# Optimization experiments

Measured on AMD Instinct MI355X. Metric: run time of the kernel, lower is better.

## Reference

```python
import jax, jax.numpy as jnp
import numpy as np

N = 50000
E = 800000
IN_C, HID_C, OUT_C = 128, 128, 64


def setup_inputs() -> dict:
    key = jax.random.key(0)
    k1, k2, k3, k4 = jax.random.split(key, 4)
    x = jax.random.normal(k1, (N, IN_C), dtype=jnp.float32)
    edge_index = jax.random.randint(k2, (2, E), 0, N, dtype=jnp.int32)
    # Glorot-ish init for the two linear layers (PyG GCNConv uses glorot)
    W1 = jax.random.normal(k3, (IN_C, HID_C), dtype=jnp.float32) / np.sqrt(IN_C)
    b1 = jnp.zeros((HID_C,), dtype=jnp.float32)
    W2 = jax.random.normal(k4, (HID_C, OUT_C), dtype=jnp.float32) / np.sqrt(HID_C)
    b2 = jnp.zeros((OUT_C,), dtype=jnp.float32)
    return {"x": x, "edge_index": edge_index, "W1": W1, "b1": b1, "W2": W2, "b2": b2}


def _gcn_norm(edge_index, num_nodes):
    # Add self-loops, then symmetric normalization deg^{-1/2}[row]*deg^{-1/2}[col]
    loop = jnp.arange(num_nodes, dtype=edge_index.dtype)
    row = jnp.concatenate([edge_index[0], loop])  # [E+N] source
    col = jnp.concatenate([edge_index[1], loop])  # [E+N] destination
    deg = jax.ops.segment_sum(jnp.ones_like(col, dtype=jnp.float32), col,
                              num_segments=num_nodes)
    deg_isqrt = jax.lax.rsqrt(deg)  # deg >= 1 due to self-loops
    norm = deg_isqrt[row] * deg_isqrt[col]  # [E+N]
    return row, col, norm


def _gcn_conv(x, row, col, norm, W, b, num_nodes):
    x = x @ W                                   # [N, C_out]
    msg = x[row] * norm[:, None]                # gather + scale, [E+N, C_out]
    out = jax.ops.segment_sum(msg, col, num_segments=num_nodes)  # scatter-add
    return out + b


def reference(x, edge_index, W1, b1, W2, b2):
    num_nodes = x.shape[0]
    row, col, norm = _gcn_norm(edge_index, num_nodes)
    h = _gcn_conv(x, row, col, norm, W1, b1, num_nodes)
    h = jax.nn.relu(h)
    out = _gcn_conv(h, row, col, norm, W2, b2, num_nodes)
    return out
```

## Files before the change

kernel.cpp:

```cpp
#include <hip/hip_runtime.h>


typedef float f32x4 __attribute__((ext_vector_type(4)));
typedef short bf16x8 __attribute__((ext_vector_type(8)));

#define EPB 4096

__device__ inline float bf2f(unsigned short u) {
    return __uint_as_float(((unsigned int)u) << 16);
}
__device__ inline unsigned short f2bf(float f) {
    unsigned int x = __float_as_uint(f);
    x = x + 0x7FFFu + ((x >> 16) & 1u);
    return (unsigned short)(x >> 16);
}
__device__ inline float4 cvt4(ushort4 u) {
    return make_float4(bf2f(u.x), bf2f(u.y), bf2f(u.z), bf2f(u.w));
}

__global__ __launch_bounds__(256) void k_rhist(const int* __restrict__ col,
                                               int* __restrict__ hist,
                                               int e, int nbR, int nbB) {
    __shared__ int h[256];
    int t = threadIdx.x;
    h[t] = 0;
    __syncthreads();
    int base = blockIdx.x * EPB;
#pragma unroll
    for (int i = 0; i < EPB / 256; ++i) {
        int idx = base + t + i * 256;
        if (idx < e) atomicAdd(&h[col[idx] >> 8], 1);
    }
    __syncthreads();
    if (t < nbB) hist[t * nbR + blockIdx.x] = h[t];
}

__global__ __launch_bounds__(256) void k_scan1g(const int* __restrict__ src,
                                                int* __restrict__ dst,
                                                int* __restrict__ bsum, int m) {
    __shared__ int s[256];
    int t = threadIdx.x;
    int i = blockIdx.x * 256 + t;
    int v = (i < m) ? src[i] : 0;
    s[t] = v;
    __syncthreads();
#pragma unroll
    for (int off = 1; off < 256; off <<= 1) {
        int u = (t >= off) ? s[t - off] : 0;
        __syncthreads();
        s[t] += u;
        __syncthreads();
    }
    if (i < m) dst[i] = s[t] - v;
    if (t == 255) bsum[blockIdx.x] = s[255];
}

__global__ __launch_bounds__(256) void k_scan2(int* __restrict__ bsum, int nb) {
    __shared__ int s[256];
    int t = threadIdx.x;
    int v = (t < nb) ? bsum[t] : 0;
    s[t] = v;
    __syncthreads();
#pragma unroll
    for (int off = 1; off < 256; off <<= 1) {
        int u = (t >= off) ? s[t - off] : 0;
        __syncthreads();
        s[t] += u;
        __syncthreads();
    }
    if (t < nb) bsum[t] = s[t] - v;
}

__global__ __launch_bounds__(256) void k_scanaddg(int* __restrict__ dst,
                                                  const int* __restrict__ bsum, int m) {
    int i = blockIdx.x * 256 + threadIdx.x;
    if (i < m) dst[i] += bsum[blockIdx.x];
}

__global__ __launch_bounds__(256) void k_rscatter(const int* __restrict__ row,
                                                  const int* __restrict__ col,
                                                  const int* __restrict__ histscan,
                                                  unsigned int* __restrict__ tmp,
                                                  int e, int nbR, int nbB) {
    __shared__ int base[256];
    __shared__ int h[256];
    int t = threadIdx.x;
    base[t] = (t < nbB) ? histscan[t * nbR + blockIdx.x] : 0;
    h[t] = 0;
    __syncthreads();
    int b0 = blockIdx.x * EPB;
#pragma unroll
    for (int i = 0; i < EPB / 256; ++i) {
        int idx = b0 + t + i * 256;
        if (idx < e) {
            int c = col[idx];
            int bin = c >> 8;
            int rk = atomicAdd(&h[bin], 1);
            tmp[base[bin] + rk] =
                ((unsigned int)(c & 255) << 16) | (unsigned int)row[idx];
        }
    }
}

__global__ __launch_bounds__(256) void k_bsort(const unsigned int* __restrict__ tmp,
                                               const int* __restrict__ histscan,
                                               int* __restrict__ indptr,
                                               float* __restrict__ dinv,
                                               unsigned short* __restrict__ srcidx,
                                               int n, int e, int nbR, int nbB) {
    __shared__ int cnt[256];
    __shared__ int pre[256];
    int b = blockIdx.x;
    int t = threadIdx.x;
    int beg = histscan[b * nbR];
    int end = (b + 1 < nbB) ? histscan[(b + 1) * nbR] : e;

    cnt[t] = 0;
    __syncthreads();
    for (int i = beg + t; i < end; i += 256) atomicAdd(&cnt[tmp[i] >> 16], 1);
    __syncthreads();
    int v = cnt[t];
    pre[t] = v;
    __syncthreads();
#pragma unroll
    for (int off = 1; off < 256; off <<= 1) {
        int u = (t >= off) ? pre[t - off] : 0;
        __syncthreads();
        pre[t] += u;
        __syncthreads();
    }
    int myexcl = pre[t] - v;
    int node = b * 256 + t;
    if (node < n) {
        indptr[node] = beg + myexcl;
        dinv[node] = rsqrtf((float)v + 1.0f);
    }
    if (b == nbB - 1 && t == 0) indptr[n] = e;
    __syncthreads();
    pre[t] = beg + myexcl;
    cnt[t] = 0;
    __syncthreads();
    for (int i = beg + t; i < end; i += 256) {
        unsigned int u = tmp[i];
        int cl = u >> 16;
        int rk = atomicAdd(&cnt[cl], 1);
        srcidx[pre[cl] + rk] = (unsigned short)(u & 0xFFFFu);
    }
}

__global__ __launch_bounds__(256) void k_prepw(const float* __restrict__ W1,
                                               const float* __restrict__ W2,
                                               unsigned short* __restrict__ Wt1,
                                               unsigned short* __restrict__ Wt2) {
    int i = blockIdx.x * 256 + threadIdx.x;
    if (i < 16384) {
        int k = i >> 7, nc = i & 127;
        Wt1[nc * 128 + k] = f2bf(W1[i]);
    } else if (i < 16384 + 8192) {
        int i2 = i - 16384;
        int k = i2 >> 6, nc = i2 & 63;
        Wt2[nc * 128 + k] = f2bf(W2[i2]);
    }
}

__global__ __launch_bounds__(256, 2) void k_gemm1(const float* __restrict__ x,
                                                  const unsigned short* __restrict__ Wt,
                                                  const float* __restrict__ dinv,
                                                  unsigned short* __restrict__ hs, int n) {
    __shared__ unsigned short Xs[128 * 136];
    __shared__ unsigned short Ws[128 * 136];
    __shared__ float dinv_s[128];
    int t = threadIdx.x;
    int r0blk = blockIdx.x * 128;

#pragma unroll
    for (int i = 0; i < 8; ++i) {
        int c = t + i * 256;
        int nc = c >> 4;
        int k0 = (c & 15) * 8;
        bf16x8 v = *(const bf16x8*)&Wt[nc * 128 + k0];
        *(bf16x8*)&Ws[nc * 136 + k0] = v;
    }
#pragma unroll
    for (int i = 0; i < 16; ++i) {
        int c = t + i * 256;
        int r = c >> 5;
        int kq = c & 31;
        float4 v = make_float4(0.f, 0.f, 0.f, 0.f);
        int gr = r0blk + r;
        if (gr < n) v = ((const float4*)x)[gr * 32 + kq];
        ushort4 o;
        o.x = f2bf(v.x); o.y = f2bf(v.y); o.z = f2bf(v.z); o.w = f2bf(v.w);
        *(ushort4*)&Xs[r * 136 + kq * 4] = o;
    }
    if (t < 128) {
        int gr = r0blk + t;
        dinv_s[t] = (gr < n) ? dinv[gr] : 0.f;
    }
    __syncthreads();

    int lane = t & 63, wave = t >> 6;
    int lrow = lane & 15;
    int lk = (lane >> 4) * 8;

    f32x4 acc[2][8];
#pragma unroll
    for (int mi = 0; mi < 2; ++mi)
#pragma unroll
        for (int ni = 0; ni < 8; ++ni) acc[mi][ni] = (f32x4){0.f, 0.f, 0.f, 0.f};

#pragma unroll
    for (int ks = 0; ks < 4; ++ks) {
        int kk = ks * 32 + lk;
        bf16x8 a0 = *(bf16x8*)&Xs[(wave * 32 + lrow) * 136 + kk];
        bf16x8 a1 = *(bf16x8*)&Xs[(wave * 32 + 16 + lrow) * 136 + kk];
#pragma unroll
        for (int ni = 0; ni < 8; ++ni) {
            bf16x8 b = *(bf16x8*)&Ws[(ni * 16 + lrow) * 136 + kk];
            acc[0][ni] = __builtin_amdgcn_mfma_f32_16x16x32_bf16(a0, b, acc[0][ni], 0, 0, 0);
            acc[1][ni] = __builtin_amdgcn_mfma_f32_16x16x32_bf16(a1, b, acc[1][ni], 0, 0, 0);
        }
    }

    int rq = (lane >> 4) * 4;
#pragma unroll
    for (int mi = 0; mi < 2; ++mi)
#pragma unroll
        for (int r = 0; r < 4; ++r) {
            int lrw = wave * 32 + mi * 16 + rq + r;
            int grow = r0blk + lrw;
            if (grow < n) {
                float dv = dinv_s[lrw];
#pragma unroll
                for (int ni = 0; ni < 8; ++ni)
                    hs[grow * 128 + ni * 16 + lrow] = f2bf(acc[mi][ni][r] * dv);
            }
        }
}

__global__ __launch_bounds__(256) void k_gather1(const int* __restrict__ indptr,
                                                 const unsigned short* __restrict__ srcidx,
                                                 const unsigned short* __restrict__ hs,
                                                 const float* __restrict__ dinv,
                                                 const float* __restrict__ b1,
                                                 unsigned short* __restrict__ h1, int n) {
    int wid = (blockIdx.x * 256 + threadIdx.x) >> 6;
    if (wid >= n) return;
    int lane = threadIdx.x & 63;
    int half = lane >> 5;
    int hl = lane & 31;
    const ushort4* hv = (const ushort4*)hs;

    int beg = indptr[wid], end = indptr[wid + 1];
    float4 a0 = make_float4(0.f, 0.f, 0.f, 0.f), a1 = a0, a2 = a0, a3 = a0;

    int j = beg;
    for (; j + 7 < end; j += 8) {
        int sA = srcidx[j + half];
        int sB = srcidx[j + 2 + half];
        int sC = srcidx[j + 4 + half];
        int sD = srcidx[j + 6 + half];
        float4 v;
        v = cvt4(hv[sA * 32 + hl]); a0.x += v.x; a0.y += v.y; a0.z += v.z; a0.w += v.w;
        v = cvt4(hv[sB * 32 + hl]); a1.x += v.x; a1.y += v.y; a1.z += v.z; a1.w += v.w;
        v = cvt4(hv[sC * 32 + hl]); a2.x += v.x; a2.y += v.y; a2.z += v.z; a2.w += v.w;
        v = cvt4(hv[sD * 32 + hl]); a3.x += v.x; a3.y += v.y; a3.z += v.z; a3.w += v.w;
    }
    if (j + half < end) {
        float4 v = cvt4(hv[srcidx[j + half] * 32 + hl]);
        a0.x += v.x; a0.y += v.y; a0.z += v.z; a0.w += v.w;
    }
    j += 2;
    if (j + half < end) {
        float4 v = cvt4(hv[srcidx[j + half] * 32 + hl]);
        a1.x += v.x; a1.y += v.y; a1.z += v.z; a1.w += v.w;
    }
    j += 2;
    if (j + half < end) {
        float4 v = cvt4(hv[srcidx[j + half] * 32 + hl]);
        a2.x += v.x; a2.y += v.y; a2.z += v.z; a2.w += v.w;
    }
    j += 2;
    if (j + half < end) {
        float4 v = cvt4(hv[srcidx[j + half] * 32 + hl]);
        a3.x += v.x; a3.y += v.y; a3.z += v.z; a3.w += v.w;
    }

    float4 sv = cvt4(hv[wid * 32 + hl]);
    if (half == 0) {
        a0.x += sv.x; a0.y += sv.y; a0.z += sv.z; a0.w += sv.w;
    }

    float4 tsum;
    tsum.x = a0.x + a1.x + a2.x + a3.x;
    tsum.y = a0.y + a1.y + a2.y + a3.y;
    tsum.z = a0.z + a1.z + a2.z + a3.z;
    tsum.w = a0.w + a1.w + a2.w + a3.w;
    tsum.x += __shfl_xor(tsum.x, 32);
    tsum.y += __shfl_xor(tsum.y, 32);
    tsum.z += __shfl_xor(tsum.z, 32);
    tsum.w += __shfl_xor(tsum.w, 32);

    if (half == 0) {
        float d = dinv[wid];
        float4 bb = *(const float4*)&b1[hl * 4];
        ushort4 o;
        o.x = f2bf(fmaxf(tsum.x * d + bb.x, 0.f));
        o.y = f2bf(fmaxf(tsum.y * d + bb.y, 0.f));
        o.z = f2bf(fmaxf(tsum.z * d + bb.z, 0.f));
        o.w = f2bf(fmaxf(tsum.w * d + bb.w, 0.f));
        ((ushort4*)h1)[wid * 32 + hl] = o;
    }
}

__global__ __launch_bounds__(256, 3) void k_gemm2(const unsigned short* __restrict__ h1,
                                                  const unsigned short* __restrict__ Wt,
                                                  const float* __restrict__ dinv,
                                                  unsigned short* __restrict__ ps2, int n) {
    __shared__ unsigned short Xs[128 * 136];
    __shared__ unsigned short Ws[64 * 136];
    __shared__ float dinv_s[128];
    int t = threadIdx.x;
    int r0blk = blockIdx.x * 128;

#pragma unroll
    for (int i = 0; i < 4; ++i) {
        int c = t + i * 256;
        int nc = c >> 4;
        int k0 = (c & 15) * 8;
        bf16x8 v = *(const bf16x8*)&Wt[nc * 128 + k0];
        *(bf16x8*)&Ws[nc * 136 + k0] = v;
    }
#pragma unroll
    for (int i = 0; i < 8; ++i) {
        int c = t + i * 256;
        int r = c >> 4;
        int k0 = (c & 15) * 8;
        int gr = r0blk + r;
        bf16x8 v = (bf16x8)(short)0;
        if (gr < n) v = *(const bf16x8*)&h1[gr * 128 + k0];
        *(bf16x8*)&Xs[r * 136 + k0] = v;
    }
    if (t < 128) {
        int gr = r0blk + t;
        dinv_s[t] = (gr < n) ? dinv[gr] : 0.f;
    }
    __syncthreads();

    int lane = t & 63, wave = t >> 6;
    int lrow = lane & 15;
    int lk = (lane >> 4) * 8;

    f32x4 acc[2][4];
#pragma unroll
    for (int mi = 0; mi < 2; ++mi)
#pragma unroll
        for (int ni = 0; ni < 4; ++ni) acc[mi][ni] = (f32x4){0.f, 0.f, 0.f, 0.f};

#pragma unroll
    for (int ks = 0; ks < 4; ++ks) {
        int kk = ks * 32 + lk;
        bf16x8 a0 = *(bf16x8*)&Xs[(wave * 32 + lrow) * 136 + kk];
        bf16x8 a1 = *(bf16x8*)&Xs[(wave * 32 + 16 + lrow) * 136 + kk];
#pragma unroll
        for (int ni = 0; ni < 4; ++ni) {
            bf16x8 b = *(bf16x8*)&Ws[(ni * 16 + lrow) * 136 + kk];
            acc[0][ni] = __builtin_amdgcn_mfma_f32_16x16x32_bf16(a0, b, acc[0][ni], 0, 0, 0);
            acc[1][ni] = __builtin_amdgcn_mfma_f32_16x16x32_bf16(a1, b, acc[1][ni], 0, 0, 0);
        }
    }

    int rq = (lane >> 4) * 4;
#pragma unroll
    for (int mi = 0; mi < 2; ++mi)
#pragma unroll
        for (int r = 0; r < 4; ++r) {
            int lrw = wave * 32 + mi * 16 + rq + r;
            int grow = r0blk + lrw;
            if (grow < n) {
                float dv = dinv_s[lrw];
#pragma unroll
                for (int ni = 0; ni < 4; ++ni)
                    ps2[grow * 64 + ni * 16 + lrow] = f2bf(acc[mi][ni][r] * dv);
            }
        }
}

__global__ __launch_bounds__(256) void k_gather2(const int* __restrict__ indptr,
                                                 const unsigned short* __restrict__ srcidx,
                                                 const unsigned short* __restrict__ ps2,
                                                 const float* __restrict__ dinv,
                                                 const float* __restrict__ b2,
                                                 float* __restrict__ out, int n) {
    int wid = (blockIdx.x * 256 + threadIdx.x) >> 6;
    if (wid >= n) return;
    int lane = threadIdx.x & 63;
    int half = lane >> 5;
    int hl = lane & 31;
    const unsigned int* pv = (const unsigned int*)ps2;

    int beg = indptr[wid], end = indptr[wid + 1];
    float2 a0 = make_float2(0.f, 0.f), a1 = a0, a2 = a0, a3 = a0;

    int j = beg;
    for (; j + 7 < end; j += 8) {
        int sA = srcidx[j + half];
        int sB = srcidx[j + 2 + half];
        int sC = srcidx[j + 4 + half];
        int sD = srcidx[j + 6 + half];
        unsigned int uA = pv[sA * 32 + hl];
        unsigned int uB = pv[sB * 32 + hl];
        unsigned int uC = pv[sC * 32 + hl];
        unsigned int uD = pv[sD * 32 + hl];
        a0.x += bf2f((unsigned short)uA); a0.y += bf2f((unsigned short)(uA >> 16));
        a1.x += bf2f((unsigned short)uB); a1.y += bf2f((unsigned short)(uB >> 16));
        a2.x += bf2f((unsigned short)uC); a2.y += bf2f((unsigned short)(uC >> 16));
        a3.x += bf2f((unsigned short)uD); a3.y += bf2f((unsigned short)(uD >> 16));
    }
    if (j + half < end) {
        unsigned int u = pv[srcidx[j + half] * 32 + hl];
        a0.x += bf2f((unsigned short)u); a0.y += bf2f((unsigned short)(u >> 16));
    }
    j += 2;
    if (j + half < end) {
        unsigned int u = pv[srcidx[j + half] * 32 + hl];
        a1.x += bf2f((unsigned short)u); a1.y += bf2f((unsigned short)(u >> 16));
    }
    j += 2;
    if (j + half < end) {
        unsigned int u = pv[srcidx[j + half] * 32 + hl];
        a2.x += bf2f((unsigned short)u); a2.y += bf2f((unsigned short)(u >> 16));
    }
    j += 2;
    if (j + half < end) {
        unsigned int u = pv[srcidx[j + half] * 32 + hl];
        a3.x += bf2f((unsigned short)u); a3.y += bf2f((unsigned short)(u >> 16));
    }

    unsigned int us = pv[wid * 32 + hl];
    if (half == 0) {
        a0.x += bf2f((unsigned short)us); a0.y += bf2f((unsigned short)(us >> 16));
    }

    float2 tsum;
    tsum.x = a0.x + a1.x + a2.x + a3.x;
    tsum.y = a0.y + a1.y + a2.y + a3.y;
    tsum.x += __shfl_xor(tsum.x, 32);
    tsum.y += __shfl_xor(tsum.y, 32);

    if (half == 0) {
        float d = dinv[wid];
        float2 bb = *(const float2*)&b2[hl * 2];
        float2 o;
        o.x = tsum.x * d + bb.x;
        o.y = tsum.y * d + bb.y;
        ((float2*)out)[wid * 32 + hl] = o;
    }
}

extern "C" void kernel_launch(void* const* d_in, const int* in_sizes, int n_in,
                              void* d_out, int out_size, void* d_ws, size_t ws_size,
                              hipStream_t stream) {
    const float* x  = (const float*)d_in[0];
    const int*   ei = (const int*)d_in[1];
    const float* W1 = (const float*)d_in[2];
    const float* b1 = (const float*)d_in[3];
    const float* W2 = (const float*)d_in[4];
    const float* b2 = (const float*)d_in[5];
    float* out = (float*)d_out;

    int n = in_sizes[0] / 128;
    int e = in_sizes[1] / 2;
    const int* row = ei;
    const int* col = ei + e;

    int nbR = (e + EPB - 1) / EPB;
    int nbB = (n + 255) / 256;
    int m   = nbB * nbR;

    int* iw = (int*)d_ws;
    size_t o = 0;
    int* hist     = iw + o; o += (size_t)m;        o = (o + 3) & ~(size_t)3;
    int* histscan = iw + o; o += (size_t)m;        o = (o + 3) & ~(size_t)3;
    int* bsum     = iw + o; o += 256;
    int* indptr   = iw + o; o += (size_t)(n + 1);  o = (o + 3) & ~(size_t)3;
    float* dinv   = (float*)(iw + o); o += (size_t)n; o = (o + 3) & ~(size_t)3;
    unsigned int* tmp = (unsigned int*)(iw + o); o += (size_t)e; o = (o + 3) & ~(size_t)3;
    unsigned short* srcidx = (unsigned short*)(iw + o); o += (size_t)(e / 2 + 2); o = (o + 3) & ~(size_t)3;
    unsigned short* Wt1 = (unsigned short*)(iw + o); o += 8192;
    unsigned short* Wt2 = (unsigned short*)(iw + o); o += 4096;
    unsigned short* hs  = (unsigned short*)(iw + o);
    unsigned short* h1  = hs + (size_t)n * 128;
    unsigned short* ps2 = hs;

    int nbm = (m + 255) / 256;

    k_rhist<<<nbR, 256, 0, stream>>>(col, hist, e, nbR, nbB);
    k_scan1g<<<nbm, 256, 0, stream>>>(hist, histscan, bsum, m);
    k_scan2<<<1, 256, 0, stream>>>(bsum, nbm);
    k_scanaddg<<<nbm, 256, 0, stream>>>(histscan, bsum, m);
    k_rscatter<<<nbR, 256, 0, stream>>>(row, col, histscan, tmp, e, nbR, nbB);
    k_bsort<<<nbB, 256, 0, stream>>>(tmp, histscan, indptr, dinv, srcidx, n, e, nbR, nbB);
    k_prepw<<<96, 256, 0, stream>>>(W1, W2, Wt1, Wt2);

    int nbg = (n + 127) / 128;
    k_gemm1<<<nbg, 256, 0, stream>>>(x, Wt1, dinv, hs, n);
    k_gather1<<<(n * 64 + 255) / 256, 256, 0, stream>>>(indptr, srcidx, hs, dinv, b1, h1, n);
    k_gemm2<<<nbg, 256, 0, stream>>>(h1, Wt2, dinv, ps2, n);
    k_gather2<<<(n * 64 + 255) / 256, 256, 0, stream>>>(indptr, srcidx, ps2, dinv, b2, out, n);
}
```

Baseline: 136.1 us.

## Slice feature matrices into 32-column panels and shrink CSR build launches

Intermediate bf16 feature matrices are stored as 32-column slices (64 bytes per row). The gather kernels process one slice per block group, so each gather pass works on a smaller, more cache-resident footprint, and each wave handles four edges at a time with 16 lanes per row. The CSR build replaces the global multi-kernel scan with per-bucket atomic counters plus a single small scan, and folds the weight transpose into the histogram kernel, cutting kernel launches. The cost is an extra init launch, nondeterministic bucket-offset ordering from atomics, and narrower 4-byte loads per lane in the gathers.

```diff
diff --git a/kernel.cpp b/kernel.cpp
--- a/kernel.cpp
+++ b/kernel.cpp
@@ -14,13 +14,31 @@
     x = x + 0x7FFFu + ((x >> 16) & 1u);
     return (unsigned short)(x >> 16);
 }
-__device__ inline float4 cvt4(ushort4 u) {
-    return make_float4(bf2f(u.x), bf2f(u.y), bf2f(u.z), bf2f(u.w));
+
+__global__ __launch_bounds__(256) void k_init(int* __restrict__ bucket_cnt) {
+    bucket_cnt[threadIdx.x] = 0;
 }
 
 __global__ __launch_bounds__(256) void k_rhist(const int* __restrict__ col,
-                                               int* __restrict__ hist,
+                                               int* __restrict__ bbase,
+                                               int* __restrict__ bucket_cnt,
+                                               const float* __restrict__ W1,
+                                               const float* __restrict__ W2,
+                                               unsigned short* __restrict__ Wt1,
+                                               unsigned short* __restrict__ Wt2,
                                                int e, int nbR, int nbB) {
+    if ((int)blockIdx.x >= nbR) {
+        int i = ((int)blockIdx.x - nbR) * 256 + threadIdx.x;
+        if (i < 16384) {
+            int k = i >> 7, nc = i & 127;
+            Wt1[nc * 128 + k] = f2bf(W1[i]);
+        } else if (i < 24576) {
+            int i2 = i - 16384;
+            int k = i2 >> 6, nc = i2 & 63;
+            Wt2[nc * 128 + k] = f2bf(W2[i2]);
+        }
+        return;
+    }
     __shared__ int h[256];
     int t = threadIdx.x;
     h[t] = 0;
@@ -32,16 +50,14 @@
         if (idx < e) atomicAdd(&h[col[idx] >> 8], 1);
     }
     __syncthreads();
-    if (t < nbB) hist[t * nbR + blockIdx.x] = h[t];
-}
-
-__global__ __launch_bounds__(256) void k_scan1g(const int* __restrict__ src,
-                                                int* __restrict__ dst,
-                                                int* __restrict__ bsum, int m) {
+    if (t < nbB) bbase[t * nbR + blockIdx.x] = atomicAdd(&bucket_cnt[t], h[t]);
+}
+
+__global__ __launch_bounds__(256) void k_scanB(const int* __restrict__ bucket_cnt,
+                                               int* __restrict__ bucket_base, int nbB) {
     __shared__ int s[256];
     int t = threadIdx.x;
-    int i = blockIdx.x * 256 + t;
-    int v = (i < m) ? src[i] : 0;
+    int v = (t < nbB) ? bucket_cnt[t] : 0;
     s[t] = v;
     __syncthreads();
 #pragma unroll
@@ -51,41 +67,20 @@
         s[t] += u;
         __syncthreads();
     }
-    if (i < m) dst[i] = s[t] - v;
-    if (t == 255) bsum[blockIdx.x] = s[255];
-}
-
-__global__ __launch_bounds__(256) void k_scan2(int* __restrict__ bsum, int nb) {
-    __shared__ int s[256];
-    int t = threadIdx.x;
-    int v = (t < nb) ? bsum[t] : 0;
-    s[t] = v;
-    __syncthreads();
-#pragma unroll
-    for (int off = 1; off < 256; off <<= 1) {
-        int u = (t >= off) ? s[t - off] : 0;
-        __syncthreads();
-        s[t] += u;
-        __syncthreads();
-    }
-    if (t < nb) bsum[t] = s[t] - v;
-}
-
-__global__ __launch_bounds__(256) void k_scanaddg(int* __restrict__ dst,
-                                                  const int* __restrict__ bsum, int m) {
-    int i = blockIdx.x * 256 + threadIdx.x;
-    if (i < m) dst[i] += bsum[blockIdx.x];
+    if (t < nbB) bucket_base[t] = s[t] - v;
+    if (t == 255) bucket_base[nbB] = s[255];
 }
 
 __global__ __launch_bounds__(256) void k_rscatter(const int* __restrict__ row,
                                                   const int* __restrict__ col,
-                                                  const int* __restrict__ histscan,
+                                                  const int* __restrict__ bucket_base,
+                                                  const int* __restrict__ bbase,
                                                   unsigned int* __restrict__ tmp,
                                                   int e, int nbR, int nbB) {
     __shared__ int base[256];
     __shared__ int h[256];
     int t = threadIdx.x;
-    base[t] = (t < nbB) ? histscan[t * nbR + blockIdx.x] : 0;
+    base[t] = (t < nbB) ? bucket_base[t] + bbase[t * nbR + blockIdx.x] : 0;
     h[t] = 0;
     __syncthreads();
     int b0 = blockIdx.x * EPB;
@@ -103,17 +98,17 @@
 }
 
 __global__ __launch_bounds__(256) void k_bsort(const unsigned int* __restrict__ tmp,
-                                               const int* __restrict__ histscan,
+                                               const int* __restrict__ bucket_base,
                                                int* __restrict__ indptr,
                                                float* __restrict__ dinv,
                                                unsigned short* __restrict__ srcidx,
-                                               int n, int e, int nbR, int nbB) {
+                                               int n, int e, int nbB) {
     __shared__ int cnt[256];
     __shared__ int pre[256];
     int b = blockIdx.x;
     int t = threadIdx.x;
-    int beg = histscan[b * nbR];
-    int end = (b + 1 < nbB) ? histscan[(b + 1) * nbR] : e;
+    int beg = bucket_base[b];
+    int end = bucket_base[b + 1];
 
     cnt[t] = 0;
     __syncthreads();
@@ -145,21 +140,6 @@
         int cl = u >> 16;
         int rk = atomicAdd(&cnt[cl], 1);
         srcidx[pre[cl] + rk] = (unsigned short)(u & 0xFFFFu);
-    }
-}
-
-__global__ __launch_bounds__(256) void k_prepw(const float* __restrict__ W1,
-                                               const float* __restrict__ W2,
-                                               unsigned short* __restrict__ Wt1,
-                                               unsigned short* __restrict__ Wt2) {
-    int i = blockIdx.x * 256 + threadIdx.x;
-    if (i < 16384) {
-        int k = i >> 7, nc = i & 127;
-        Wt1[nc * 128 + k] = f2bf(W1[i]);
-    } else if (i < 16384 + 8192) {
-        int i2 = i - 16384;
-        int k = i2 >> 6, nc = i2 & 63;
-        Wt2[nc * 128 + k] = f2bf(W2[i2]);
     }
 }
 
@@ -223,6 +203,7 @@
     }
 
     int rq = (lane >> 4) * 4;
+    size_t ns32 = (size_t)n * 32;
 #pragma unroll
     for (int mi = 0; mi < 2; ++mi)
 #pragma unroll
@@ -233,83 +214,62 @@
                 float dv = dinv_s[lrw];
 #pragma unroll
                 for (int ni = 0; ni < 8; ++ni)
-                    hs[grow * 128 + ni * 16 + lrow] = f2bf(acc[mi][ni][r] * dv);
+                    hs[(size_t)(ni >> 1) * ns32 + (size_t)grow * 32 + (ni & 1) * 16 + lrow] =
+                        f2bf(acc[mi][ni][r] * dv);
             }
         }
 }
 
-__global__ __launch_bounds__(256) void k_gather1(const int* __restrict__ indptr,
-                                                 const unsigned short* __restrict__ srcidx,
-                                                 const unsigned short* __restrict__ hs,
-                                                 const float* __restrict__ dinv,
-                                                 const float* __restrict__ b1,
-                                                 unsigned short* __restrict__ h1, int n) {
-    int wid = (blockIdx.x * 256 + threadIdx.x) >> 6;
-    if (wid >= n) return;
+__global__ __launch_bounds__(256) void k_gather1s(const int* __restrict__ indptr,
+                                                  const unsigned short* __restrict__ srcidx,
+                                                  const unsigned short* __restrict__ hs,
+                                                  const float* __restrict__ dinv,
+                                                  const float* __restrict__ b1,
+                                                  unsigned short* __restrict__ h1,
+                                                  int n, int nbn) {
+    int s = blockIdx.x / nbn;
+    int node = (blockIdx.x % nbn) * 4 + (threadIdx.x >> 6);
+    if (node >= n) return;
     int lane = threadIdx.x & 63;
-    int half = lane >> 5;
-    int hl = lane & 31;
-    const ushort4* hv = (const ushort4*)hs;
-
-    int beg = indptr[wid], end = indptr[wid + 1];
-    float4 a0 = make_float4(0.f, 0.f, 0.f, 0.f), a1 = a0, a2 = a0, a3 = a0;
-
+    int es = lane >> 4, cp = lane & 15;
+    const unsigned int* hv = (const unsigned int*)(hs + (size_t)s * n * 32);
+
+    int beg = indptr[node], end = indptr[node + 1];
+    float2 a0 = make_float2(0.f, 0.f), a1 = a0;
     int j = beg;
     for (; j + 7 < end; j += 8) {
-        int sA = srcidx[j + half];
-        int sB = srcidx[j + 2 + half];
-        int sC = srcidx[j + 4 + half];
-        int sD = srcidx[j + 6 + half];
-        float4 v;
-        v = cvt4(hv[sA * 32 + hl]); a0.x += v.x; a0.y += v.y; a0.z += v.z; a0.w += v.w;
-        v = cvt4(hv[sB * 32 + hl]); a1.x += v.x; a1.y += v.y; a1.z += v.z; a1.w += v.w;
-        v = cvt4(hv[sC * 32 + hl]); a2.x += v.x; a2.y += v.y; a2.z += v.z; a2.w += v.w;
-        v = cvt4(hv[sD * 32 + hl]); a3.x += v.x; a3.y += v.y; a3.z += v.z; a3.w += v.w;
-    }
-    if (j + half < end) {
-        float4 v = cvt4(hv[srcidx[j + half] * 32 + hl]);
-        a0.x += v.x; a0.y += v.y; a0.z += v.z; a0.w += v.w;
-    }
-    j += 2;
-    if (j + half < end) {
-        float4 v = cvt4(hv[srcidx[j + half] * 32 + hl]);
-        a1.x += v.x; a1.y += v.y; a1.z += v.z; a1.w += v.w;
-    }
-    j += 2;
-    if (j + half < end) {
-        float4 v = cvt4(hv[srcidx[j + half] * 32 + hl]);
-        a2.x += v.x; a2.y += v.y; a2.z += v.z; a2.w += v.w;
-    }
-    j += 2;
-    if (j + half < end) {
-        float4 v = cvt4(hv[srcidx[j + half] * 32 + hl]);
-        a3.x += v.x; a3.y += v.y; a3.z += v.z; a3.w += v.w;
-    }
-
-    float4 sv = cvt4(hv[wid * 32 + hl]);
-    if (half == 0) {
-        a0.x += sv.x; a0.y += sv.y; a0.z += sv.z; a0.w += sv.w;
-    }
-
-    float4 tsum;
-    tsum.x = a0.x + a1.x + a2.x + a3.x;
-    tsum.y = a0.y + a1.y + a2.y + a3.y;
-    tsum.z = a0.z + a1.z + a2.z + a3.z;
-    tsum.w = a0.w + a1.w + a2.w + a3.w;
-    tsum.x += __shfl_xor(tsum.x, 32);
-    tsum.y += __shfl_xor(tsum.y, 32);
-    tsum.z += __shfl_xor(tsum.z, 32);
-    tsum.w += __shfl_xor(tsum.w, 32);
-
-    if (half == 0) {
-        float d = dinv[wid];
-        float4 bb = *(const float4*)&b1[hl * 4];
-        ushort4 o;
-        o.x = f2bf(fmaxf(tsum.x * d + bb.x, 0.f));
-        o.y = f2bf(fmaxf(tsum.y * d + bb.y, 0.f));
-        o.z = f2bf(fmaxf(tsum.z * d + bb.z, 0.f));
-        o.w = f2bf(fmaxf(tsum.w * d + bb.w, 0.f));
-        ((ushort4*)h1)[wid * 32 + hl] = o;
+        int s0 = srcidx[j + es];
+        int s1 = srcidx[j + 4 + es];
+        unsigned int u0 = hv[s0 * 16 + cp];
+        unsigned int u1 = hv[s1 * 16 + cp];
+        a0.x += bf2f((unsigned short)u0); a0.y += bf2f((unsigned short)(u0 >> 16));
+        a1.x += bf2f((unsigned short)u1); a1.y += bf2f((unsigned short)(u1 >> 16));
+    }
+    if (j + 3 < end) {
+        unsigned int u = hv[srcidx[j + es] * 16 + cp];
+        a0.x += bf2f((unsigned short)u); a0.y += bf2f((unsigned short)(u >> 16));
+        j += 4;
+    }
+    if (j + es < end) {
+        unsigned int u = hv[srcidx[j + es] * 16 + cp];
+        a1.x += bf2f((unsigned short)u); a1.y += bf2f((unsigned short)(u >> 16));
+    }
+    if (es == 0) {
+        unsigned int u = hv[node * 16 + cp];
+        a0.x += bf2f((unsigned short)u); a0.y += bf2f((unsigned short)(u >> 16));
+    }
+    float2 t2;
+    t2.x = a0.x + a1.x;
+    t2.y = a0.y + a1.y;
+    t2.x += __shfl_xor(t2.x, 16); t2.x += __shfl_xor(t2.x, 32);
+    t2.y += __shfl_xor(t2.y, 16); t2.y += __shfl_xor(t2.y, 32);
+
+    if (lane < 16) {
+        float d = dinv[node];
+        float2 bb = *(const float2*)&b1[s * 32 + cp * 2];
+        unsigned int o = ((unsigned int)f2bf(fmaxf(t2.y * d + bb.y, 0.f)) << 16) |
+                         (unsigned int)f2bf(fmaxf(t2.x * d + bb.x, 0.f));
+        ((unsigned int*)h1)[(size_t)s * n * 16 + (size_t)node * 16 + cp] = o;
     }
 }
 
@@ -322,6 +282,7 @@
     __shared__ float dinv_s[128];
     int t = threadIdx.x;
     int r0blk = blockIdx.x * 128;
+    size_t ns32 = (size_t)n * 32;
 
 #pragma unroll
     for (int i = 0; i < 4; ++i) {
@@ -338,7 +299,7 @@
         int k0 = (c & 15) * 8;
         int gr = r0blk + r;
         bf16x8 v = (bf16x8)(short)0;
-        if (gr < n) v = *(const bf16x8*)&h1[gr * 128 + k0];
+        if (gr < n) v = *(const bf16x8*)&h1[(size_t)(k0 >> 5) * ns32 + (size_t)gr * 32 + (k0 & 31)];
         *(bf16x8*)&Xs[r * 136 + k0] = v;
     }
     if (t < 128) {
@@ -381,80 +342,63 @@
                 float dv = dinv_s[lrw];
 #pragma unroll
                 for (int ni = 0; ni < 4; ++ni)
-                    ps2[grow * 64 + ni * 16 + lrow] = f2bf(acc[mi][ni][r] * dv);
+                    ps2[(size_t)(ni >> 1) * ns32 + (size_t)grow * 32 + (ni & 1) * 16 + lrow] =
+                        f2bf(acc[mi][ni][r] * dv);
             }
         }
 }
 
-__global__ __launch_bounds__(256) void k_gather2(const int* __restrict__ indptr,
-                                                 const unsigned short* __restrict__ srcidx,
-                                                 const unsigned short* __restrict__ ps2,
-                                                 const float* __restrict__ dinv,
-                                                 const float* __restrict__ b2,
-                                                 float* __restrict__ out, int n) {
-    int wid = (blockIdx.x * 256 + threadIdx.x) >> 6;
-    if (wid >= n) return;
+__global__ __launch_bounds__(256) void k_gather2s(const int* __restrict__ indptr,
+                                                  const unsigned short* __restrict__ srcidx,
+                                                  const unsigned short* __restrict__ ps2,
+                                                  const float* __restrict__ dinv,
+                                                  const float* __restrict__ b2,
+                                                  float* __restrict__ out,
+                                                  int n, int nbn) {
+    int s = blockIdx.x / nbn;
+    int node = (blockIdx.x % nbn) * 4 + (threadIdx.x >> 6);
+    if (node >= n) return;
     int lane = threadIdx.x & 63;
-    int half = lane >> 5;
-    int hl = lane & 31;
-    const unsigned int* pv = (const unsigned int*)ps2;
-
-    int beg = indptr[wid], end = indptr[wid + 1];
-    float2 a0 = make_float2(0.f, 0.f), a1 = a0, a2 = a0, a3 = a0;
-
+    int es = lane >> 4, cp = lane & 15;
+    const unsigned int* pv = (const unsigned int*)(ps2 + (size_t)s * n * 32);
+
+    int beg = indptr[node], end = indptr[node + 1];
+    float2 a0 = make_float2(0.f, 0.f), a1 = a0;
     int j = beg;
     for (; j + 7 < end; j += 8) {
-        int sA = srcidx[j + half];
-        int sB = srcidx[j + 2 + half];
-        int sC = srcidx[j + 4 + half];
-        int sD = srcidx[j + 6 + half];
-        unsigned int uA = pv[sA * 32 + hl];
-        unsigned int uB = pv[sB * 32 + hl];
-        unsigned int uC = pv[sC * 32 + hl];
-        unsigned int uD = pv[sD * 32 + hl];
-        a0.x += bf2f((unsigned short)uA); a0.y += bf2f((unsigned short)(uA >> 16));
-        a1.x += bf2f((unsigned short)uB); a1.y += bf2f((unsigned short)(uB >> 16));
-        a2.x += bf2f((unsigned short)uC); a2.y += bf2f((unsigned short)(uC >> 16));
-        a3.x += bf2f((unsigned short)uD); a3.y += bf2f((unsigned short)(uD >> 16));
-    }
-    if (j + half < end) {
-        unsigned int u = pv[srcidx[j + half] * 32 + hl];
+        int s0 = srcidx[j + es];
+        int s1 = srcidx[j + 4 + es];
+        unsigned int u0 = pv[s0 * 16 + cp];
+        unsigned int u1 = pv[s1 * 16 + cp];
+        a0.x += bf2f((unsigned short)u0); a0.y += bf2f((unsigned short)(u0 >> 16));
+        a1.x += bf2f((unsigned short)u1); a1.y += bf2f((unsigned short)(u1 >> 16));
+    }
+    if (j + 3 < end) {
+        unsigned int u = pv[srcidx[j + es] * 16 + cp];
         a0.x += bf2f((unsigned short)u); a0.y += bf2f((unsigned short)(u >> 16));
-    }
-    j += 2;
-    if (j + half < end) {
-        unsigned int u = pv[srcidx[j + half] * 32 + hl];
+        j += 4;
+    }
+    if (j + es < end) {
+        unsigned int u = pv[srcidx[j + es] * 16 + cp];
         a1.x += bf2f((unsigned short)u); a1.y += bf2f((unsigned short)(u >> 16));
     }
-    j += 2;
-    if (j + half < end) {
-        unsigned int u = pv[srcidx[j + half] * 32 + hl];
-        a2.x += bf2f((unsigned short)u); a2.y += bf2f((unsigned short)(u >> 16));
-    }
-    j += 2;
-    if (j + half < end) {
-        unsigned int u = pv[srcidx[j + half] * 32 + hl];
-        a3.x += bf2f((unsigned short)u); a3.y += bf2f((unsigned short)(u >> 16));
-    }
-
-    unsigned int us = pv[wid * 32 + hl];
-    if (half == 0) {
-        a0.x += bf2f((unsigned short)us); a0.y += bf2f((unsigned short)(us >> 16));
-    }
-
-    float2 tsum;
-    tsum.x = a0.x + a1.x + a2.x + a3.x;
-    tsum.y = a0.y + a1.y + a2.y + a3.y;
-    tsum.x += __shfl_xor(tsum.x, 32);
-    tsum.y += __shfl_xor(tsum.y, 32);
-
-    if (half == 0) {
-        float d = dinv[wid];
-        float2 bb = *(const float2*)&b2[hl * 2];
+    if (es == 0) {
+        unsigned int u = pv[node * 16 + cp];
+        a0.x += bf2f((unsigned short)u); a0.y += bf2f((unsigned short)(u >> 16));
+    }
+    float2 t2;
+    t2.x = a0.x + a1.x;
+    t2.y = a0.y + a1.y;
+    t2.x += __shfl_xor(t2.x, 16); t2.x += __shfl_xor(t2.x, 32);
+    t2.y += __shfl_xor(t2.y, 16); t2.y += __shfl_xor(t2.y, 32);
+
+    if (lane < 16) {
+        float d = dinv[node];
+        float2 bb = *(const float2*)&b2[s * 32 + cp * 2];
         float2 o;
-        o.x = tsum.x * d + bb.x;
-        o.y = tsum.y * d + bb.y;
-        ((float2*)out)[wid * 32 + hl] = o;
+        o.x = t2.x * d + bb.x;
+        o.y = t2.y * d + bb.y;
+        ((float2*)out)[(size_t)node * 32 + s * 16 + cp] = o;
     }
 }
 
@@ -480,11 +424,11 @@
 
     int* iw = (int*)d_ws;
     size_t o = 0;
-    int* hist     = iw + o; o += (size_t)m;        o = (o + 3) & ~(size_t)3;
-    int* histscan = iw + o; o += (size_t)m;        o = (o + 3) & ~(size_t)3;
-    int* bsum     = iw + o; o += 256;
-    int* indptr   = iw + o; o += (size_t)(n + 1);  o = (o + 3) & ~(size_t)3;
-    float* dinv   = (float*)(iw + o); o += (size_t)n; o = (o + 3) & ~(size_t)3;
+    int* bucket_cnt  = iw + o; o += 256;
+    int* bucket_base = iw + o; o += 256;
+    int* bbase       = iw + o; o += (size_t)m;           o = (o + 3) & ~(size_t)3;
+    int* indptr      = iw + o; o += (size_t)(n + 1);     o = (o + 3) & ~(size_t)3;
+    float* dinv      = (float*)(iw + o); o += (size_t)n; o = (o + 3) & ~(size_t)3;
     unsigned int* tmp = (unsigned int*)(iw + o); o += (size_t)e; o = (o + 3) & ~(size_t)3;
     unsigned short* srcidx = (unsigned short*)(iw + o); o += (size_t)(e / 2 + 2); o = (o + 3) & ~(size_t)3;
     unsigned short* Wt1 = (unsigned short*)(iw + o); o += 8192;
@@ -493,19 +437,16 @@
     unsigned short* h1  = hs + (size_t)n * 128;
     unsigned short* ps2 = hs;
 
-    int nbm = (m + 255) / 256;
-
-    k_rhist<<<nbR, 256, 0, stream>>>(col, hist, e, nbR, nbB);
-    k_scan1g<<<nbm, 256, 0, stream>>>(hist, histscan, bsum, m);
-    k_scan2<<<1, 256, 0, stream>>>(bsum, nbm);
-    k_scanaddg<<<nbm, 256, 0, stream>>>(histscan, bsum, m);
-    k_rscatter<<<nbR, 256, 0, stream>>>(row, col, histscan, tmp, e, nbR, nbB);
-    k_bsort<<<nbB, 256, 0, stream>>>(tmp, histscan, indptr, dinv, srcidx, n, e, nbR, nbB);
-    k_prepw<<<96, 256, 0, stream>>>(W1, W2, Wt1, Wt2);
+    k_init<<<1, 256, 0, stream>>>(bucket_cnt);
+    k_rhist<<<nbR + 96, 256, 0, stream>>>(col, bbase, bucket_cnt, W1, W2, Wt1, Wt2, e, nbR, nbB);
+    k_scanB<<<1, 256, 0, stream>>>(bucket_cnt, bucket_base, nbB);
+    k_rscatter<<<nbR, 256, 0, stream>>>(row, col, bucket_base, bbase, tmp, e, nbR, nbB);
+    k_bsort<<<nbB, 256, 0, stream>>>(tmp, bucket_base, indptr, dinv, srcidx, n, e, nbB);
 
     int nbg = (n + 127) / 128;
+    int nbn = (n + 3) / 4;
     k_gemm1<<<nbg, 256, 0, stream>>>(x, Wt1, dinv, hs, n);
-    k_gather1<<<(n * 64 + 255) / 256, 256, 0, stream>>>(indptr, srcidx, hs, dinv, b1, h1, n);
+    k_gather1s<<<4 * nbn, 256, 0, stream>>>(indptr, srcidx, hs, dinv, b1, h1, n, nbn);
     k_gemm2<<<nbg, 256, 0, stream>>>(h1, Wt2, dinv, ps2, n);
-    k_gather2<<<(n * 64 + 255) / 256, 256, 0, stream>>>(indptr, srcidx, ps2, dinv, b2, out, n);
-}
+    k_gather2s<<<2 * nbn, 256, 0, stream>>>(indptr, srcidx, ps2, dinv, b2, out, n, nbn);
+}
```

After: 188.4 us. +38.4%, slower.

## Replace multi-pass histogram scan with atomic bucket offsets and fuse weight prep

Applied to the files above, without the earlier changes.

Each histogram block now claims its slot inside each bucket with a global atomicAdd on per-bucket counters. This replaces the three-kernel global exclusive scan over the bucket-by-block matrix with a single small bucket scan. The weight transpose and bf16 conversion is folded into extra blocks of the histogram kernel. Together these cut the launch count from seven to four kernels plus a memset. In exchange, the order of blocks within a bucket becomes nondeterministic, so neighbour order within each CSR row can vary between runs.

```diff
diff --git a/kernel.cpp b/kernel.cpp
--- a/kernel.cpp
+++ b/kernel.cpp
@@ -19,8 +19,25 @@
 }
 
 __global__ __launch_bounds__(256) void k_rhist(const int* __restrict__ col,
-                                               int* __restrict__ hist,
+                                               int* __restrict__ bbase,
+                                               int* __restrict__ bucket_cnt,
+                                               const float* __restrict__ W1,
+                                               const float* __restrict__ W2,
+                                               unsigned short* __restrict__ Wt1,
+                                               unsigned short* __restrict__ Wt2,
                                                int e, int nbR, int nbB) {
+    if ((int)blockIdx.x >= nbR) {
+        int i = ((int)blockIdx.x - nbR) * 256 + threadIdx.x;
+        if (i < 16384) {
+            int k = i >> 7, nc = i & 127;
+            Wt1[nc * 128 + k] = f2bf(W1[i]);
+        } else if (i < 24576) {
+            int i2 = i - 16384;
+            int k = i2 >> 6, nc = i2 & 63;
+            Wt2[nc * 128 + k] = f2bf(W2[i2]);
+        }
+        return;
+    }
     __shared__ int h[256];
     int t = threadIdx.x;
     h[t] = 0;
@@ -32,16 +49,14 @@
         if (idx < e) atomicAdd(&h[col[idx] >> 8], 1);
     }
     __syncthreads();
-    if (t < nbB) hist[t * nbR + blockIdx.x] = h[t];
-}
-
-__global__ __launch_bounds__(256) void k_scan1g(const int* __restrict__ src,
-                                                int* __restrict__ dst,
-                                                int* __restrict__ bsum, int m) {
+    if (t < nbB) bbase[t * nbR + blockIdx.x] = atomicAdd(&bucket_cnt[t], h[t]);
+}
+
+__global__ __launch_bounds__(256) void k_scanB(const int* __restrict__ bucket_cnt,
+                                               int* __restrict__ bucket_base, int nbB) {
     __shared__ int s[256];
     int t = threadIdx.x;
-    int i = blockIdx.x * 256 + t;
-    int v = (i < m) ? src[i] : 0;
+    int v = (t < nbB) ? bucket_cnt[t] : 0;
     s[t] = v;
     __syncthreads();
 #pragma unroll
@@ -51,41 +66,20 @@
         s[t] += u;
         __syncthreads();
     }
-    if (i < m) dst[i] = s[t] - v;
-    if (t == 255) bsum[blockIdx.x] = s[255];
-}
-
-__global__ __launch_bounds__(256) void k_scan2(int* __restrict__ bsum, int nb) {
-    __shared__ int s[256];
-    int t = threadIdx.x;
-    int v = (t < nb) ? bsum[t] : 0;
-    s[t] = v;
-    __syncthreads();
-#pragma unroll
-    for (int off = 1; off < 256; off <<= 1) {
-        int u = (t >= off) ? s[t - off] : 0;
-        __syncthreads();
-        s[t] += u;
-        __syncthreads();
-    }
-    if (t < nb) bsum[t] = s[t] - v;
-}
-
-__global__ __launch_bounds__(256) void k_scanaddg(int* __restrict__ dst,
-                                                  const int* __restrict__ bsum, int m) {
-    int i = blockIdx.x * 256 + threadIdx.x;
-    if (i < m) dst[i] += bsum[blockIdx.x];
+    if (t < nbB) bucket_base[t] = s[t] - v;
+    if (t == 255) bucket_base[nbB] = s[255];
 }
 
 __global__ __launch_bounds__(256) void k_rscatter(const int* __restrict__ row,
                                                   const int* __restrict__ col,
-                                                  const int* __restrict__ histscan,
+                                                  const int* __restrict__ bucket_base,
+                                                  const int* __restrict__ bbase,
                                                   unsigned int* __restrict__ tmp,
                                                   int e, int nbR, int nbB) {
     __shared__ int base[256];
     __shared__ int h[256];
     int t = threadIdx.x;
-    base[t] = (t < nbB) ? histscan[t * nbR + blockIdx.x] : 0;
+    base[t] = (t < nbB) ? bucket_base[t] + bbase[t * nbR + blockIdx.x] : 0;
     h[t] = 0;
     __syncthreads();
     int b0 = blockIdx.x * EPB;
@@ -103,17 +97,17 @@
 }
 
 __global__ __launch_bounds__(256) void k_bsort(const unsigned int* __restrict__ tmp,
-                                               const int* __restrict__ histscan,
+                                               const int* __restrict__ bucket_base,
                                                int* __restrict__ indptr,
                                                float* __restrict__ dinv,
                                                unsigned short* __restrict__ srcidx,
-                                               int n, int e, int nbR, int nbB) {
+                                               int n, int e, int nbB) {
     __shared__ int cnt[256];
     __shared__ int pre[256];
     int b = blockIdx.x;
     int t = threadIdx.x;
-    int beg = histscan[b * nbR];
-    int end = (b + 1 < nbB) ? histscan[(b + 1) * nbR] : e;
+    int beg = bucket_base[b];
+    int end = bucket_base[b + 1];
 
     cnt[t] = 0;
     __syncthreads();
@@ -145,21 +139,6 @@
         int cl = u >> 16;
         int rk = atomicAdd(&cnt[cl], 1);
         srcidx[pre[cl] + rk] = (unsigned short)(u & 0xFFFFu);
-    }
-}
-
-__global__ __launch_bounds__(256) void k_prepw(const float* __restrict__ W1,
-                                               const float* __restrict__ W2,
-                                               unsigned short* __restrict__ Wt1,
-                                               unsigned short* __restrict__ Wt2) {
-    int i = blockIdx.x * 256 + threadIdx.x;
-    if (i < 16384) {
-        int k = i >> 7, nc = i & 127;
-        Wt1[nc * 128 + k] = f2bf(W1[i]);
-    } else if (i < 16384 + 8192) {
-        int i2 = i - 16384;
-        int k = i2 >> 6, nc = i2 & 63;
-        Wt2[nc * 128 + k] = f2bf(W2[i2]);
     }
 }
 
@@ -480,11 +459,11 @@
 
     int* iw = (int*)d_ws;
     size_t o = 0;
-    int* hist     = iw + o; o += (size_t)m;        o = (o + 3) & ~(size_t)3;
-    int* histscan = iw + o; o += (size_t)m;        o = (o + 3) & ~(size_t)3;
-    int* bsum     = iw + o; o += 256;
-    int* indptr   = iw + o; o += (size_t)(n + 1);  o = (o + 3) & ~(size_t)3;
-    float* dinv   = (float*)(iw + o); o += (size_t)n; o = (o + 3) & ~(size_t)3;
+    int* bucket_cnt  = iw + o; o += 256;
+    int* bucket_base = iw + o; o += 256;
+    int* bbase       = iw + o; o += (size_t)m;           o = (o + 3) & ~(size_t)3;
+    int* indptr      = iw + o; o += (size_t)(n + 1);     o = (o + 3) & ~(size_t)3;
+    float* dinv      = (float*)(iw + o); o += (size_t)n; o = (o + 3) & ~(size_t)3;
     unsigned int* tmp = (unsigned int*)(iw + o); o += (size_t)e; o = (o + 3) & ~(size_t)3;
     unsigned short* srcidx = (unsigned short*)(iw + o); o += (size_t)(e / 2 + 2); o = (o + 3) & ~(size_t)3;
     unsigned short* Wt1 = (unsigned short*)(iw + o); o += 8192;
@@ -493,15 +472,11 @@
     unsigned short* h1  = hs + (size_t)n * 128;
     unsigned short* ps2 = hs;
 
-    int nbm = (m + 255) / 256;
-
-    k_rhist<<<nbR, 256, 0, stream>>>(col, hist, e, nbR, nbB);
-    k_scan1g<<<nbm, 256, 0, stream>>>(hist, histscan, bsum, m);
-    k_scan2<<<1, 256, 0, stream>>>(bsum, nbm);
-    k_scanaddg<<<nbm, 256, 0, stream>>>(histscan, bsum, m);
-    k_rscatter<<<nbR, 256, 0, stream>>>(row, col, histscan, tmp, e, nbR, nbB);
-    k_bsort<<<nbB, 256, 0, stream>>>(tmp, histscan, indptr, dinv, srcidx, n, e, nbR, nbB);
-    k_prepw<<<96, 256, 0, stream>>>(W1, W2, Wt1, Wt2);
+    hipMemsetAsync(bucket_cnt, 0, 256 * sizeof(int), stream);
+    k_rhist<<<nbR + 96, 256, 0, stream>>>(col, bbase, bucket_cnt, W1, W2, Wt1, Wt2, e, nbR, nbB);
+    k_scanB<<<1, 256, 0, stream>>>(bucket_cnt, bucket_base, nbB);
+    k_rscatter<<<nbR, 256, 0, stream>>>(row, col, bucket_base, bbase, tmp, e, nbR, nbB);
+    k_bsort<<<nbB, 256, 0, stream>>>(tmp, bucket_base, indptr, dinv, srcidx, n, e, nbB);
 
     int nbg = (n + 127) / 128;
     k_gemm1<<<nbg, 256, 0, stream>>>(x, Wt1, dinv, hs, n);
```

Result: no change. 136.5 us (+0.3%).
